# Optimization experiments

Hardware: AMD Instinct MI355X
Metric: run time of the kernel (lower is better)

Reference implementation:

```python
import jax, jax.numpy as jnp
import numpy as np
from jax import lax

B, FEA, C, DIM_OUT, HEADS, H, W = 4, 3, 256, 256, 8, 32, 32
EPS = 1e-5


def setup_inputs() -> dict:
    key = jax.random.key(0)
    ks = jax.random.split(key, 10)
    return {
        "x": jax.random.normal(ks[0], (B, C, H, W), jnp.float32),
        "query": jax.random.normal(ks[1], (B, FEA * H * W, C), jnp.float32),
        "conv_q_w": jax.random.normal(ks[2], (FEA, C, 1, 3, 3), jnp.float32) * 0.1,
        "bn_q_gamma": jnp.ones((FEA, C), jnp.float32),
        "bn_q_beta": jnp.zeros((FEA, C), jnp.float32),
        "bn_q_mean": jnp.zeros((FEA, C), jnp.float32),
        "bn_q_var": jnp.ones((FEA, C), jnp.float32),
        "conv_k_w": jax.random.normal(ks[3], (C, 1, 3, 3), jnp.float32) * 0.1,
        "bn_k_gamma": jnp.ones((C,), jnp.float32),
        "bn_k_beta": jnp.zeros((C,), jnp.float32),
        "bn_k_mean": jnp.zeros((C,), jnp.float32),
        "bn_k_var": jnp.ones((C,), jnp.float32),
        "conv_v_w": jax.random.normal(ks[4], (C, 1, 3, 3), jnp.float32) * 0.1,
        "bn_v_gamma": jnp.ones((C,), jnp.float32),
        "bn_v_beta": jnp.zeros((C,), jnp.float32),
        "bn_v_mean": jnp.zeros((C,), jnp.float32),
        "bn_v_var": jnp.ones((C,), jnp.float32),
        "proj_q_w": jax.random.normal(ks[5], (DIM_OUT, C), jnp.float32) * 0.02,
        "proj_k_w": jax.random.normal(ks[6], (DIM_OUT, C), jnp.float32) * 0.02,
        "proj_v_w": jax.random.normal(ks[7], (DIM_OUT, C), jnp.float32) * 0.02,
        "proj_w": jax.random.normal(ks[8], (DIM_OUT, DIM_OUT), jnp.float32) * 0.02,
        "proj_b": jnp.zeros((DIM_OUT,), jnp.float32),
        "h": H,
        "w": W,
    }


def _dw_conv_bn(x, w, gamma, beta, mean, var):
    # x: [B, C, H, W]; w: [C, 1, 3, 3] depthwise; BN in eval mode (running stats)
    y = lax.conv_general_dilated(
        x, w, window_strides=(1, 1), padding="SAME",
        feature_group_count=x.shape[1],
        dimension_numbers=("NCHW", "OIHW", "NCHW"))
    inv = gamma * lax.rsqrt(var + EPS)
    return y * inv[None, :, None, None] + (beta - mean * inv)[None, :, None, None]


def reference(x, query, conv_q_w, bn_q_gamma, bn_q_beta, bn_q_mean, bn_q_var,
              conv_k_w, bn_k_gamma, bn_k_beta, bn_k_mean, bn_k_var,
              conv_v_w, bn_v_gamma, bn_v_beta, bn_v_mean, bn_v_var,
              proj_q_w, proj_k_w, proj_v_w, proj_w, proj_b, h, w):
    b, c = x.shape[0], x.shape[1]
    res = h * w
    # split query into fea_no maps, depthwise conv + BN each, concat tokens
    q_parts = []
    for i in range(FEA):
        qi = query[:, res * i:res * (i + 1), :].reshape(b, h, w, c).transpose(0, 3, 1, 2)
        qi = _dw_conv_bn(qi, conv_q_w[i], bn_q_gamma[i], bn_q_beta[i], bn_q_mean[i], bn_q_var[i])
        q_parts.append(qi.reshape(b, c, res).transpose(0, 2, 1))  # [B, h*w, C]
    q_tok = jnp.concatenate(q_parts, axis=1)                      # [B, FEA*h*w, C]
    k_tok = _dw_conv_bn(x, conv_k_w, bn_k_gamma, bn_k_beta, bn_k_mean, bn_k_var)
    k_tok = k_tok.reshape(b, c, res).transpose(0, 2, 1)           # [B, h*w, C]
    v_tok = _dw_conv_bn(x, conv_v_w, bn_v_gamma, bn_v_beta, bn_v_mean, bn_v_var)
    v_tok = v_tok.reshape(b, c, res).transpose(0, 2, 1)
    hd = DIM_OUT // HEADS
    q = (q_tok @ proj_q_w.T).reshape(b, -1, HEADS, hd).transpose(0, 2, 1, 3)  # [B,H,L,d]
    k = (k_tok @ proj_k_w.T).reshape(b, -1, HEADS, hd).transpose(0, 2, 1, 3)  # [B,H,T,d]
    v = (v_tok @ proj_v_w.T).reshape(b, -1, HEADS, hd).transpose(0, 2, 1, 3)
    scale = DIM_OUT ** (-0.5)  # note: original scales by dim_out, not head_dim
    attn = jax.nn.softmax(jnp.einsum("bhld,bhtd->bhlt", q, k) * scale, axis=-1)
    out = jnp.einsum("bhlt,bhtd->bhld", attn, v)
    out = out.transpose(0, 2, 1, 3).reshape(b, -1, DIM_OUT)
    return out @ proj_w.T + proj_b
```

## Files before the change

kernel.cpp:

```cpp
#include <hip/hip_runtime.h>
#include <hip/hip_bf16.h>
#include <math.h>

#define B_     4
#define C_     256
#define RES_   1024
#define FEA_   3
#define LQ_    3072
#define HEADS_ 8
#define EPS_   1e-5f

typedef __bf16 bf16x8 __attribute__((ext_vector_type(8)));
typedef float  f32x16 __attribute__((ext_vector_type(16)));
typedef unsigned int uint4e __attribute__((ext_vector_type(4)));

#if __has_builtin(__builtin_amdgcn_exp2f)
#define EXP2(x) __builtin_amdgcn_exp2f(x)
#else
#define EXP2(x) exp2f(x)
#endif

__device__ __forceinline__ unsigned short bfbits(float v) {
    return __builtin_bit_cast(unsigned short, (__bf16)v);
}
__device__ __forceinline__ unsigned int pkbf(float lo, float hi2) {
    return (unsigned int)bfbits(lo) | ((unsigned int)bfbits(hi2) << 16);
}

__global__ __launch_bounds__(256) void pre_kernel(
    const float* __restrict__ query, const float* __restrict__ x,
    const float* __restrict__ wq,
    const float* __restrict__ gq, const float* __restrict__ bq,
    const float* __restrict__ mq, const float* __restrict__ vq,
    const float* __restrict__ wk, const float* __restrict__ gk, const float* __restrict__ bk,
    const float* __restrict__ mk, const float* __restrict__ vk,
    const float* __restrict__ wv, const float* __restrict__ gv, const float* __restrict__ bv,
    const float* __restrict__ mv, const float* __restrict__ vv,
    const float* __restrict__ pw0, const float* __restrict__ pw1,
    const float* __restrict__ pw2, const float* __restrict__ pw3,
    __bf16* __restrict__ q_tok, float* __restrict__ k_tok, float* __restrict__ v_tok,
    __bf16* __restrict__ Wq, __bf16* __restrict__ Wk,
    __bf16* __restrict__ Wv, __bf16* __restrict__ Wo)
{
    __shared__ float plane[RES_];
    int blk = blockIdx.x, tid = threadIdx.x;

    if (blk < 768) {
        int b = blk / 192, rem = blk % 192;
        int part = rem >> 6, t = rem & 63;
        int y0 = (t >> 3) * 4, x0 = (t & 7) * 4;
        int c = tid;
        const float* wp = wq + (size_t)(part * 256 + c) * 9;
        const float* qb = query + ((size_t)b * LQ_ + (size_t)part * 1024) * 256 + c;

        float w[9];
#pragma unroll
        for (int i = 0; i < 9; ++i) w[i] = wp[i];

        float v[6][6];
#pragma unroll
        for (int iy = 0; iy < 6; ++iy) {
            int yy = y0 - 1 + iy;
#pragma unroll
            for (int ix = 0; ix < 6; ++ix) {
                int xx = x0 - 1 + ix;
                bool ok = ((unsigned)yy < 32u) && ((unsigned)xx < 32u);
                v[iy][ix] = ok ? qb[(size_t)(yy * 32 + xx) * 256] : 0.f;
            }
        }
        int gi = part * 256 + c;
        float inv = gq[gi] * rsqrtf(vq[gi] + EPS_);
        float sh  = bq[gi] - mq[gi] * inv;
#pragma unroll
        for (int yi = 0; yi < 4; ++yi) {
#pragma unroll
            for (int xi = 0; xi < 4; ++xi) {
                float acc = 0.f;
#pragma unroll
                for (int ky = 0; ky < 3; ++ky)
#pragma unroll
                    for (int kj = 0; kj < 3; ++kj)
                        acc = fmaf(w[ky * 3 + kj], v[yi + ky][xi + kj], acc);
                int l = part * 1024 + (y0 + yi) * 32 + x0 + xi;
                q_tok[((size_t)b * LQ_ + l) * 256 + c] = (__bf16)fmaf(acc, inv, sh);
            }
        }
    } else if (blk < 2816) {
        int idx = blk - 768;
        int c = idx & 255, b = (idx >> 8) & 3, which = idx >> 10;
        const float* xp = x + ((size_t)b * 256 + c) * RES_;
#pragma unroll
        for (int i = 0; i < 4; ++i) plane[tid + i * 256] = xp[tid + i * 256];
        __syncthreads();

        const float* wp = (which ? wv : wk) + (size_t)c * 9;
        float w[9];
#pragma unroll
        for (int i = 0; i < 9; ++i) w[i] = wp[i];
        float inv = (which ? gv : gk)[c] * rsqrtf((which ? vv : vk)[c] + EPS_);
        float sh  = (which ? bv : bk)[c] - (which ? mv : mk)[c] * inv;
        float* out = (which ? v_tok : k_tok) + ((size_t)b * 256 + c) * RES_;
#pragma unroll
        for (int i0 = 0; i0 < 4; ++i0) {
            int p = tid + i0 * 256;
            int y = p >> 5, xx = p & 31;
            float acc = 0.f;
#pragma unroll
            for (int ky = 0; ky < 3; ++ky) {
                int yy = y + ky - 1;
                if ((unsigned)yy >= 32u) continue;
#pragma unroll
                for (int kx = 0; kx < 3; ++kx) {
                    int x2 = xx + kx - 1;
                    if ((unsigned)x2 >= 32u) continue;
                    acc = fmaf(w[ky * 3 + kx], plane[yy * 32 + x2], acc);
                }
            }
            out[p] = fmaf(acc, inv, sh);
        }
    } else {
        int idx = blk - 2816;
        int m = idx >> 6;
        const float* s = m == 0 ? pw0 : m == 1 ? pw1 : m == 2 ? pw2 : pw3;
        __bf16*      d = m == 0 ? Wq  : m == 1 ? Wk  : m == 2 ? Wv  : Wo;
        int i = ((idx & 63) * 256 + tid) * 4;
        float4 v = *(const float4*)(s + i);
        ushort4 u;
        u.x = bfbits(v.x); u.y = bfbits(v.y); u.z = bfbits(v.z); u.w = bfbits(v.w);
        *(ushort4*)(d + i) = u;
    }
}

__global__ __launch_bounds__(256) void gemm_qkv_kernel(
    const __bf16* __restrict__ qt, const float* __restrict__ kt, const float* __restrict__ vt,
    const __bf16* __restrict__ Wq, const __bf16* __restrict__ Wk, const __bf16* __restrict__ Wv,
    __bf16* __restrict__ Qb, __bf16* __restrict__ Kb, __bf16* __restrict__ VT)
{
    int tid = threadIdx.x, lane = tid & 63, l31 = lane & 31, hi = lane >> 5;
    int gid = blockIdx.x * 4 + (tid >> 6);

    f32x16 acc;
#pragma unroll
    for (int r = 0; r < 16; ++r) acc[r] = 0.f;

    if (gid < 3072) {
        int b = gid / 768, rem = gid % 768;
        int j0 = (rem >> 3) * 32, i0 = (rem & 7) * 32;
        const __bf16* Bp = qt + ((size_t)b * LQ_ + j0 + l31) * 256 + 8 * hi;
        const __bf16* Ap = Wq + (size_t)(i0 + l31) * 256 + 8 * hi;
#pragma unroll
        for (int k0 = 0; k0 < 256; k0 += 16) {
            acc = __builtin_amdgcn_mfma_f32_32x32x16_bf16(
                *(const bf16x8*)(Ap + k0), *(const bf16x8*)(Bp + k0), acc, 0, 0, 0);
        }
        const float scale = 0.0625f * 1.44269504f;
        int head = i0 >> 5;
        __bf16* op = Qb + ((size_t)(b * HEADS_ + head) * LQ_ + j0 + l31) * 32 + 4 * hi;
#pragma unroll
        for (int rr = 0; rr < 4; ++rr) {
            ushort4 u;
            u.x = bfbits(acc[4 * rr + 0] * scale); u.y = bfbits(acc[4 * rr + 1] * scale);
            u.z = bfbits(acc[4 * rr + 2] * scale); u.w = bfbits(acc[4 * rr + 3] * scale);
            *(ushort4*)(op + 8 * rr) = u;
        }
    } else if (gid < 4096) {
        int g = gid - 3072;
        int b = g >> 8, rem = g & 255;
        int j0 = (rem >> 3) * 32, i0 = (rem & 7) * 32;
        const float* Bbase = kt + (size_t)b * 256 * RES_ + j0 + l31;
        const __bf16* Ap = Wk + (size_t)(i0 + l31) * 256 + 8 * hi;
#pragma unroll
        for (int k0 = 0; k0 < 256; k0 += 16) {
            bf16x8 bfr;
#pragma unroll
            for (int jj = 0; jj < 8; ++jj)
                bfr[jj] = (__bf16)Bbase[(size_t)(k0 + 8 * hi + jj) * RES_];
            acc = __builtin_amdgcn_mfma_f32_32x32x16_bf16(
                *(const bf16x8*)(Ap + k0), bfr, acc, 0, 0, 0);
        }
        int head = i0 >> 5;
        __bf16* op = Kb + ((size_t)(b * HEADS_ + head) * RES_ + j0 + l31) * 32 + 4 * hi;
#pragma unroll
        for (int rr = 0; rr < 4; ++rr) {
            ushort4 u;
            u.x = bfbits(acc[4 * rr + 0]); u.y = bfbits(acc[4 * rr + 1]);
            u.z = bfbits(acc[4 * rr + 2]); u.w = bfbits(acc[4 * rr + 3]);
            *(ushort4*)(op + 8 * rr) = u;
        }
    } else {
        int g = gid - 4096;
        int b = g >> 8, rem = g & 255;
        int i0t = (rem >> 3) * 32, j0 = (rem & 7) * 32;
        const float* Abase = vt + (size_t)b * 256 * RES_ + i0t + l31;
        const __bf16* Bp = Wv + (size_t)(j0 + l31) * 256 + 8 * hi;
#pragma unroll
        for (int k0 = 0; k0 < 256; k0 += 16) {
            bf16x8 afr;
#pragma unroll
            for (int jj = 0; jj < 8; ++jj)
                afr[jj] = (__bf16)Abase[(size_t)(k0 + 8 * hi + jj) * RES_];
            acc = __builtin_amdgcn_mfma_f32_32x32x16_bf16(
                afr, *(const bf16x8*)(Bp + k0), acc, 0, 0, 0);
        }
        int head = j0 >> 5;
        __bf16* op = VT + ((size_t)(b * HEADS_ + head) * 32 + l31) * RES_ + i0t + 4 * hi;
#pragma unroll
        for (int rr = 0; rr < 4; ++rr) {
            ushort4 u;
            u.x = bfbits(acc[4 * rr + 0]); u.y = bfbits(acc[4 * rr + 1]);
            u.z = bfbits(acc[4 * rr + 2]); u.w = bfbits(acc[4 * rr + 3]);
            *(ushort4*)(op + 8 * rr) = u;
        }
    }
}

__global__ __launch_bounds__(256) void gemm_out_kernel(
    const __bf16* __restrict__ Oc, const __bf16* __restrict__ Wo,
    const float* __restrict__ bias, float* __restrict__ out)
{
    int tid = threadIdx.x, lane = tid & 63, l31 = lane & 31, hi = lane >> 5;
    int gid = blockIdx.x * 4 + (tid >> 6);
    int b = gid / 768, rem = gid % 768;
    int j0 = (rem >> 3) * 32, i0 = (rem & 7) * 32;
    const __bf16* Bp = Oc + ((size_t)b * LQ_ + j0 + l31) * 256 + 8 * hi;
    const __bf16* Ap = Wo + (size_t)(i0 + l31) * 256 + 8 * hi;

    f32x16 acc;
#pragma unroll
    for (int r = 0; r < 16; ++r) acc[r] = 0.f;
#pragma unroll
    for (int k0 = 0; k0 < 256; k0 += 16) {
        acc = __builtin_amdgcn_mfma_f32_32x32x16_bf16(
            *(const bf16x8*)(Ap + k0), *(const bf16x8*)(Bp + k0), acc, 0, 0, 0);
    }
    float* op = out + ((size_t)b * LQ_ + j0 + l31) * 256 + i0 + 4 * hi;
#pragma unroll
    for (int rr = 0; rr < 4; ++rr) {
        float4 bv = *(const float4*)(bias + i0 + 4 * hi + 8 * rr);
        float4 r4;
        r4.x = acc[4 * rr + 0] + bv.x; r4.y = acc[4 * rr + 1] + bv.y;
        r4.z = acc[4 * rr + 2] + bv.z; r4.w = acc[4 * rr + 3] + bv.w;
        *(float4*)(op + 8 * rr) = r4;
    }
}

__global__ __launch_bounds__(256) void attn_mfma_kernel(
    const __bf16* __restrict__ Qb, const __bf16* __restrict__ Kb,
    const __bf16* __restrict__ VT, __bf16* __restrict__ Oc)
{
    __shared__ float Os[3][64][35];
    int tid  = threadIdx.x;
    int lane = tid & 63, l31 = lane & 31, hi = lane >> 5;
    int th   = tid >> 6;

    int i    = blockIdx.x;
    int xcd  = i & 7, slot = i >> 3;
    int bh   = xcd * 4 + slot / 48;
    int q0   = (slot % 48) * 64;

    const __bf16* qpA = Qb + ((size_t)bh * LQ_ + q0 + l31) * 32 + 8 * hi;
    bf16x8 qA0 = *(const bf16x8*)qpA;
    bf16x8 qA1 = *(const bf16x8*)(qpA + 16);
    bf16x8 qB0 = *(const bf16x8*)(qpA + 1024);
    bf16x8 qB1 = *(const bf16x8*)(qpA + 1040);

    const __bf16* kp = Kb + ((size_t)bh * RES_ + th * 256 + l31) * 32 + 8 * hi;
    const __bf16* vp = VT + ((size_t)bh * 32 + l31) * RES_ + th * 256 + 8 * hi;

    f32x16 oA, oB;
#pragma unroll
    for (int r = 0; r < 16; ++r) { oA[r] = 0.f; oB[r] = 0.f; }
    float lsA = 0.f, lsB = 0.f;

    auto smpack = [&](const f32x16& s, float& ls, bf16x8& pb1, bf16x8& pb2) {
        float p[16];
#pragma unroll
        for (int r = 0; r < 16; ++r) p[r] = EXP2(s[r]);
#pragma unroll
        for (int r = 0; r < 16; ++r) ls += p[r];

        unsigned int w0 = pkbf(p[0],  p[1]),  w1 = pkbf(p[2],  p[3]);
        unsigned int w2 = pkbf(p[4],  p[5]),  w3 = pkbf(p[6],  p[7]);
        unsigned int w4 = pkbf(p[8],  p[9]),  w5 = pkbf(p[10], p[11]);
        unsigned int w6 = pkbf(p[12], p[13]), w7 = pkbf(p[14], p[15]);

        asm("v_permlane32_swap_b32 %0, %1" : "+v"(w0), "+v"(w2));
        asm("v_permlane32_swap_b32 %0, %1" : "+v"(w1), "+v"(w3));
        asm("v_permlane32_swap_b32 %0, %1" : "+v"(w4), "+v"(w6));
        asm("v_permlane32_swap_b32 %0, %1" : "+v"(w5), "+v"(w7));

        uint4e b1 = { w0, w1, w2, w3 };
        uint4e b2 = { w4, w5, w6, w7 };
        pb1 = __builtin_bit_cast(bf16x8, b1);
        pb2 = __builtin_bit_cast(bf16x8, b2);
    };

    bf16x8 kc0 = *(const bf16x8*)kp;
    bf16x8 kc1 = *(const bf16x8*)(kp + 16);

#pragma unroll
    for (int st = 0; st < 8; ++st) {
        const __bf16* vc = vp + (size_t)st * 32;
        bf16x8 V0 = *(const bf16x8*)vc;
        bf16x8 V1 = *(const bf16x8*)(vc + 16);

        bf16x8 kn0, kn1;
        if (st < 7) {
            const __bf16* kn = kp + (size_t)(st + 1) * 1024;
            kn0 = *(const bf16x8*)kn;
            kn1 = *(const bf16x8*)(kn + 16);
        }

        f32x16 sA, sB;
#pragma unroll
        for (int r = 0; r < 16; ++r) { sA[r] = 0.f; sB[r] = 0.f; }
        __builtin_amdgcn_s_setprio(1);
        sA = __builtin_amdgcn_mfma_f32_32x32x16_bf16(kc0, qA0, sA, 0, 0, 0);
        sB = __builtin_amdgcn_mfma_f32_32x32x16_bf16(kc0, qB0, sB, 0, 0, 0);
        sA = __builtin_amdgcn_mfma_f32_32x32x16_bf16(kc1, qA1, sA, 0, 0, 0);
        sB = __builtin_amdgcn_mfma_f32_32x32x16_bf16(kc1, qB1, sB, 0, 0, 0);
        __builtin_amdgcn_s_setprio(0);

        bf16x8 pA1, pA2, pB1, pB2;
        smpack(sA, lsA, pA1, pA2);
        smpack(sB, lsB, pB1, pB2);

        __builtin_amdgcn_s_setprio(1);
        oA = __builtin_amdgcn_mfma_f32_32x32x16_bf16(V0, pA1, oA, 0, 0, 0);
        oB = __builtin_amdgcn_mfma_f32_32x32x16_bf16(V0, pB1, oB, 0, 0, 0);
        oA = __builtin_amdgcn_mfma_f32_32x32x16_bf16(V1, pA2, oA, 0, 0, 0);
        oB = __builtin_amdgcn_mfma_f32_32x32x16_bf16(V1, pB2, oB, 0, 0, 0);
        __builtin_amdgcn_s_setprio(0);

        if (st < 7) { kc0 = kn0; kc1 = kn1; }
    }

    lsA += __shfl_xor(lsA, 32, 64);
    lsB += __shfl_xor(lsB, 32, 64);

    if (th) {
#pragma unroll
        for (int r = 0; r < 16; ++r) {
            Os[th - 1][lane][r]      = oA[r];
            Os[th - 1][lane][17 + r] = oB[r];
        }
        Os[th - 1][lane][16] = lsA;
        Os[th - 1][lane][33] = lsB;
    }
    __syncthreads();
    if (!th) {
        int b = bh >> 3, h = bh & 7;
        float lA = lsA + Os[0][lane][16] + Os[1][lane][16] + Os[2][lane][16];
        float lB = lsB + Os[0][lane][33] + Os[1][lane][33] + Os[2][lane][33];
        float invA = 1.0f / lA, invB = 1.0f / lB;
        __bf16* opA = Oc + ((size_t)b * LQ_ + q0 + l31) * 256 + h * 32 + 4 * hi;
        __bf16* opB = opA + (size_t)32 * 256;
#pragma unroll
        for (int rr = 0; rr < 4; ++rr) {
            ushort4 ua, ub;
            ua.x = bfbits((oA[4*rr+0] + Os[0][lane][4*rr+0] + Os[1][lane][4*rr+0] + Os[2][lane][4*rr+0]) * invA);
            ua.y = bfbits((oA[4*rr+1] + Os[0][lane][4*rr+1] + Os[1][lane][4*rr+1] + Os[2][lane][4*rr+1]) * invA);
            ua.z = bfbits((oA[4*rr+2] + Os[0][lane][4*rr+2] + Os[1][lane][4*rr+2] + Os[2][lane][4*rr+2]) * invA);
            ua.w = bfbits((oA[4*rr+3] + Os[0][lane][4*rr+3] + Os[1][lane][4*rr+3] + Os[2][lane][4*rr+3]) * invA);
            ub.x = bfbits((oB[4*rr+0] + Os[0][lane][17+4*rr+0] + Os[1][lane][17+4*rr+0] + Os[2][lane][17+4*rr+0]) * invB);
            ub.y = bfbits((oB[4*rr+1] + Os[0][lane][17+4*rr+1] + Os[1][lane][17+4*rr+1] + Os[2][lane][17+4*rr+1]) * invB);
            ub.z = bfbits((oB[4*rr+2] + Os[0][lane][17+4*rr+2] + Os[1][lane][17+4*rr+2] + Os[2][lane][17+4*rr+2]) * invB);
            ub.w = bfbits((oB[4*rr+3] + Os[0][lane][17+4*rr+3] + Os[1][lane][17+4*rr+3] + Os[2][lane][17+4*rr+3]) * invB);
            *(ushort4*)(opA + 8 * rr) = ua;
            *(ushort4*)(opB + 8 * rr) = ub;
        }
    }
}

extern "C" void kernel_launch(void* const* d_in, const int* in_sizes, int n_in,
                              void* d_out, int out_size, void* d_ws, size_t ws_size,
                              hipStream_t stream) {
    const float* x        = (const float*)d_in[0];
    const float* query    = (const float*)d_in[1];
    const float* conv_q_w = (const float*)d_in[2];
    const float* bn_q_g   = (const float*)d_in[3];
    const float* bn_q_b   = (const float*)d_in[4];
    const float* bn_q_m   = (const float*)d_in[5];
    const float* bn_q_v   = (const float*)d_in[6];
    const float* conv_k_w = (const float*)d_in[7];
    const float* bn_k_g   = (const float*)d_in[8];
    const float* bn_k_b   = (const float*)d_in[9];
    const float* bn_k_m   = (const float*)d_in[10];
    const float* bn_k_v   = (const float*)d_in[11];
    const float* conv_v_w = (const float*)d_in[12];
    const float* bn_v_g   = (const float*)d_in[13];
    const float* bn_v_b   = (const float*)d_in[14];
    const float* bn_v_m   = (const float*)d_in[15];
    const float* bn_v_v   = (const float*)d_in[16];
    const float* proj_q_w = (const float*)d_in[17];
    const float* proj_k_w = (const float*)d_in[18];
    const float* proj_v_w = (const float*)d_in[19];
    const float* proj_w   = (const float*)d_in[20];
    const float* proj_b   = (const float*)d_in[21];

    char* ws = (char*)d_ws;
    __bf16* q_tok = (__bf16*)(ws + 0);
    float*  k_tok = (float*) (ws + 6291456);
    float*  v_tok = (float*) (ws + 10485760);
    __bf16* Qb    = (__bf16*)(ws + 14680064);
    __bf16* Kb    = (__bf16*)(ws + 20971520);
    __bf16* VT    = (__bf16*)(ws + 23068672);
    __bf16* Wq    = (__bf16*)(ws + 25165824);
    __bf16* Wk    = (__bf16*)(ws + 25296896);
    __bf16* Wv    = (__bf16*)(ws + 25427968);
    __bf16* Wo    = (__bf16*)(ws + 25559040);
    __bf16* Oc    = q_tok;
    float*  out   = (float*)d_out;

    pre_kernel<<<dim3(3072), 256, 0, stream>>>(
        query, x, conv_q_w, bn_q_g, bn_q_b, bn_q_m, bn_q_v,
        conv_k_w, bn_k_g, bn_k_b, bn_k_m, bn_k_v,
        conv_v_w, bn_v_g, bn_v_b, bn_v_m, bn_v_v,
        proj_q_w, proj_k_w, proj_v_w, proj_w,
        q_tok, k_tok, v_tok, Wq, Wk, Wv, Wo);

    gemm_qkv_kernel<<<dim3(1280), 256, 0, stream>>>(
        q_tok, k_tok, v_tok, Wq, Wk, Wv, Qb, Kb, VT);

    attn_mfma_kernel<<<dim3(1536), 256, 0, stream>>>(Qb, Kb, VT, Oc);

    gemm_out_kernel<<<dim3(768), 256, 0, stream>>>(Oc, Wo, proj_b, out);
}
```

Before: 79.34 us.

## Fuse Q projection into attention kernel via LDS staging

```diff
diff --git a/kernel.cpp b/kernel.cpp
--- a/kernel.cpp
+++ b/kernel.cpp
@@ -131,10 +131,10 @@
     }
 }
 
-__global__ __launch_bounds__(256) void gemm_qkv_kernel(
-    const __bf16* __restrict__ qt, const float* __restrict__ kt, const float* __restrict__ vt,
-    const __bf16* __restrict__ Wq, const __bf16* __restrict__ Wk, const __bf16* __restrict__ Wv,
-    __bf16* __restrict__ Qb, __bf16* __restrict__ Kb, __bf16* __restrict__ VT)
+__global__ __launch_bounds__(256) void gemm_kv_kernel(
+    const float* __restrict__ kt, const float* __restrict__ vt,
+    const __bf16* __restrict__ Wk, const __bf16* __restrict__ Wv,
+    __bf16* __restrict__ Kb, __bf16* __restrict__ VT)
 {
     int tid = threadIdx.x, lane = tid & 63, l31 = lane & 31, hi = lane >> 5;
     int gid = blockIdx.x * 4 + (tid >> 6);
@@ -143,28 +143,8 @@
 #pragma unroll
     for (int r = 0; r < 16; ++r) acc[r] = 0.f;
 
-    if (gid < 3072) {
-        int b = gid / 768, rem = gid % 768;
-        int j0 = (rem >> 3) * 32, i0 = (rem & 7) * 32;
-        const __bf16* Bp = qt + ((size_t)b * LQ_ + j0 + l31) * 256 + 8 * hi;
-        const __bf16* Ap = Wq + (size_t)(i0 + l31) * 256 + 8 * hi;
-#pragma unroll
-        for (int k0 = 0; k0 < 256; k0 += 16) {
-            acc = __builtin_amdgcn_mfma_f32_32x32x16_bf16(
-                *(const bf16x8*)(Ap + k0), *(const bf16x8*)(Bp + k0), acc, 0, 0, 0);
-        }
-        const float scale = 0.0625f * 1.44269504f;
-        int head = i0 >> 5;
-        __bf16* op = Qb + ((size_t)(b * HEADS_ + head) * LQ_ + j0 + l31) * 32 + 4 * hi;
-#pragma unroll
-        for (int rr = 0; rr < 4; ++rr) {
-            ushort4 u;
-            u.x = bfbits(acc[4 * rr + 0] * scale); u.y = bfbits(acc[4 * rr + 1] * scale);
-            u.z = bfbits(acc[4 * rr + 2] * scale); u.w = bfbits(acc[4 * rr + 3] * scale);
-            *(ushort4*)(op + 8 * rr) = u;
-        }
-    } else if (gid < 4096) {
-        int g = gid - 3072;
+    if (gid < 1024) {
+        int g = gid;
         int b = g >> 8, rem = g & 255;
         int j0 = (rem >> 3) * 32, i0 = (rem & 7) * 32;
         const float* Bbase = kt + (size_t)b * 256 * RES_ + j0 + l31;
@@ -188,7 +168,7 @@
             *(ushort4*)(op + 8 * rr) = u;
         }
     } else {
-        int g = gid - 4096;
+        int g = gid - 1024;
         int b = g >> 8, rem = g & 255;
         int i0t = (rem >> 3) * 32, j0 = (rem & 7) * 32;
         const float* Abase = vt + (size_t)b * 256 * RES_ + i0t + l31;
@@ -244,11 +224,14 @@
     }
 }
 
-__global__ __launch_bounds__(256) void attn_mfma_kernel(
-    const __bf16* __restrict__ Qb, const __bf16* __restrict__ Kb,
-    const __bf16* __restrict__ VT, __bf16* __restrict__ Oc)
+__global__ __launch_bounds__(256, 4) void attn_mfma_kernel(
+    const __bf16* __restrict__ qt, const __bf16* __restrict__ Wq,
+    const __bf16* __restrict__ Kb, const __bf16* __restrict__ VT,
+    __bf16* __restrict__ Oc)
 {
     __shared__ float Os[3][64][35];
+    __shared__ __bf16 Qlds[64][40];
+
     int tid  = threadIdx.x;
     int lane = tid & 63, l31 = lane & 31, hi = lane >> 5;
     int th   = tid >> 6;
@@ -257,12 +240,36 @@
     int xcd  = i & 7, slot = i >> 3;
     int bh   = xcd * 4 + slot / 48;
     int q0   = (slot % 48) * 64;
-
-    const __bf16* qpA = Qb + ((size_t)bh * LQ_ + q0 + l31) * 32 + 8 * hi;
-    bf16x8 qA0 = *(const bf16x8*)qpA;
-    bf16x8 qA1 = *(const bf16x8*)(qpA + 16);
-    bf16x8 qB0 = *(const bf16x8*)(qpA + 1024);
-    bf16x8 qB1 = *(const bf16x8*)(qpA + 1040);
+    int b    = bh >> 3, h = bh & 7;
+
+    if (th < 2) {
+        const __bf16* Bp = qt + ((size_t)b * LQ_ + q0 + th * 32 + l31) * 256 + 8 * hi;
+        const __bf16* Ap = Wq + (size_t)(h * 32 + l31) * 256 + 8 * hi;
+        f32x16 acc;
+#pragma unroll
+        for (int r = 0; r < 16; ++r) acc[r] = 0.f;
+#pragma unroll
+        for (int k0 = 0; k0 < 256; k0 += 16) {
+            acc = __builtin_amdgcn_mfma_f32_32x32x16_bf16(
+                *(const bf16x8*)(Ap + k0), *(const bf16x8*)(Bp + k0), acc, 0, 0, 0);
+        }
+        const float scale = 0.0625f * 1.44269504f;
+        __bf16* qp = &Qlds[th * 32 + l31][4 * hi];
+#pragma unroll
+        for (int rr = 0; rr < 4; ++rr) {
+            ushort4 u;
+            u.x = bfbits(acc[4 * rr + 0] * scale); u.y = bfbits(acc[4 * rr + 1] * scale);
+            u.z = bfbits(acc[4 * rr + 2] * scale); u.w = bfbits(acc[4 * rr + 3] * scale);
+            *(ushort4*)(qp + 8 * rr) = u;
+        }
+    }
+    __syncthreads();
+
+    const __bf16* qbase = &Qlds[l31][8 * hi];
+    bf16x8 qA0 = *(const bf16x8*)qbase;
+    bf16x8 qA1 = *(const bf16x8*)(qbase + 16);
+    bf16x8 qB0 = *(const bf16x8*)(qbase + 32 * 40);
+    bf16x8 qB1 = *(const bf16x8*)(qbase + 32 * 40 + 16);
 
     const __bf16* kp = Kb + ((size_t)bh * RES_ + th * 256 + l31) * 32 + 8 * hi;
     const __bf16* vp = VT + ((size_t)bh * 32 + l31) * RES_ + th * 256 + 8 * hi;
@@ -276,8 +283,11 @@
         float p[16];
 #pragma unroll
         for (int r = 0; r < 16; ++r) p[r] = EXP2(s[r]);
-#pragma unroll
-        for (int r = 0; r < 16; ++r) ls += p[r];
+        float t0 = (p[0]+p[1]) + (p[2]+p[3]);
+        float t1 = (p[4]+p[5]) + (p[6]+p[7]);
+        float t2 = (p[8]+p[9]) + (p[10]+p[11]);
+        float t3 = (p[12]+p[13]) + (p[14]+p[15]);
+        ls += (t0 + t1) + (t2 + t3);
 
         unsigned int w0 = pkbf(p[0],  p[1]),  w1 = pkbf(p[2],  p[3]);
         unsigned int w2 = pkbf(p[4],  p[5]),  w3 = pkbf(p[6],  p[7]);
@@ -338,6 +348,7 @@
     lsA += __shfl_xor(lsA, 32, 64);
     lsB += __shfl_xor(lsB, 32, 64);
 
+    __syncthreads();
     if (th) {
 #pragma unroll
         for (int r = 0; r < 16; ++r) {
@@ -349,7 +360,6 @@
     }
     __syncthreads();
     if (!th) {
-        int b = bh >> 3, h = bh & 7;
         float lA = lsA + Os[0][lane][16] + Os[1][lane][16] + Os[2][lane][16];
         float lB = lsB + Os[0][lane][33] + Os[1][lane][33] + Os[2][lane][33];
         float invA = 1.0f / lA, invB = 1.0f / lB;
@@ -402,14 +412,13 @@
     __bf16* q_tok = (__bf16*)(ws + 0);
     float*  k_tok = (float*) (ws + 6291456);
     float*  v_tok = (float*) (ws + 10485760);
-    __bf16* Qb    = (__bf16*)(ws + 14680064);
-    __bf16* Kb    = (__bf16*)(ws + 20971520);
-    __bf16* VT    = (__bf16*)(ws + 23068672);
-    __bf16* Wq    = (__bf16*)(ws + 25165824);
-    __bf16* Wk    = (__bf16*)(ws + 25296896);
-    __bf16* Wv    = (__bf16*)(ws + 25427968);
-    __bf16* Wo    = (__bf16*)(ws + 25559040);
-    __bf16* Oc    = q_tok;
+    __bf16* Kb    = (__bf16*)(ws + 14680064);
+    __bf16* VT    = (__bf16*)(ws + 16777216);
+    __bf16* Wq    = (__bf16*)(ws + 18874368);
+    __bf16* Wk    = (__bf16*)(ws + 19005440);
+    __bf16* Wv    = (__bf16*)(ws + 19136512);
+    __bf16* Wo    = (__bf16*)(ws + 19267584);
+    __bf16* Oc    = (__bf16*)(ws + 19398656);
     float*  out   = (float*)d_out;
 
     pre_kernel<<<dim3(3072), 256, 0, stream>>>(
@@ -419,10 +428,10 @@
         proj_q_w, proj_k_w, proj_v_w, proj_w,
         q_tok, k_tok, v_tok, Wq, Wk, Wv, Wo);
 
-    gemm_qkv_kernel<<<dim3(1280), 256, 0, stream>>>(
-        q_tok, k_tok, v_tok, Wq, Wk, Wv, Qb, Kb, VT);
-
-    attn_mfma_kernel<<<dim3(1536), 256, 0, stream>>>(Qb, Kb, VT, Oc);
+    gemm_kv_kernel<<<dim3(512), 256, 0, stream>>>(
+        k_tok, v_tok, Wk, Wv, Kb, VT);
+
+    attn_mfma_kernel<<<dim3(1536), 256, 0, stream>>>(q_tok, Wq, Kb, VT, Oc);
 
     gemm_out_kernel<<<dim3(768), 256, 0, stream>>>(Oc, Wo, proj_b, out);
 }
```

After: 71.78 us. 9.5% less time.
